# Optimization experiments

Measured on AMD Instinct MI355X. Metric: run time of the kernel, lower is better.

Reference implementation:

```python
import jax, jax.numpy as jnp
import numpy as np

POOL = 7  # RoIPooling output size (7,7)


def roi_pool(x, img, rois):
    """RoIPool matching the torch loop: scale rois to feature coords, truncate to int,
    take inclusive slice [y1:y2+1, x1:x2+1] and AdaptiveMaxPool2d((7,7)).
    x: [1,C,H,W], img: [1,3,h,w], rois: [N,4] (x1,y1,x2,y2 in image coords).
    Returns [N,C,7,7]."""
    _, C, H, W = x.shape
    h_img, w_img = img.shape[2], img.shape[3]
    scale = jnp.array([W / w_img, H / h_img, W / w_img, H / h_img], jnp.float32)
    r = (rois * scale).astype(jnp.int32)  # .long() truncation (coords >= 0)
    x1 = jnp.clip(r[:, 0], 0, W - 1)
    y1 = jnp.clip(r[:, 1], 0, H - 1)
    x2 = jnp.clip(r[:, 2], 0, W - 1)
    y2 = jnp.clip(r[:, 3], 0, H - 1)
    ww = x2 - x1 + 1  # inclusive slice width
    hh = y2 - y1 + 1
    i = jnp.arange(POOL)
    # AdaptiveMaxPool bin boundaries: start=floor(i*L/7), end=ceil((i+1)*L/7)  -> [N,7]
    col_s = x1[:, None] + (i[None, :] * ww[:, None]) // POOL
    col_e = x1[:, None] + ((i[None, :] + 1) * ww[:, None] + POOL - 1) // POOL
    row_s = y1[:, None] + (i[None, :] * hh[:, None]) // POOL
    row_e = y1[:, None] + ((i[None, :] + 1) * hh[:, None] + POOL - 1) // POOL
    wpos = jnp.arange(W)
    hpos = jnp.arange(H)
    colmask = (wpos[None, None, :] >= col_s[:, :, None]) & (wpos[None, None, :] < col_e[:, :, None])  # [N,7,W]
    rowmask = (hpos[None, None, :] >= row_s[:, :, None]) & (hpos[None, None, :] < row_e[:, :, None])  # [N,7,H]
    feat = x[0]  # [C,H,W]
    neg = jnp.asarray(jnp.finfo(feat.dtype).min, feat.dtype)
    def per_roi(masks):
        rm, cm = masks  # [7,H], [7,W]
        # separable max over the rectangular bin: cols first, then rows
        t = jnp.max(jnp.where(cm[None, None, :, :], feat[:, :, None, :], neg), axis=-1)  # [C,H,7]
        return jnp.max(jnp.where(rm[None, :, :, None], t[:, None, :, :], neg), axis=2)  # [C,7,7]
    return jax.lax.map(per_roi, (rowmask, colmask))  # [N,C,7,7]


def setup_inputs() -> dict:
    key = jax.random.key(0)
    ks = jax.random.split(key, 10)
    C, H, W = 512, 50, 50
    h_img, w_img = 800, 800
    N = 512
    num_classes = 20
    x = jax.random.normal(ks[0], (1, C, H, W), jnp.float32)
    img = jnp.zeros((1, 3, h_img, w_img), jnp.float32)
    bx = jax.random.uniform(ks[1], (N,), minval=0.0, maxval=w_img - 320.0)
    by = jax.random.uniform(ks[2], (N,), minval=0.0, maxval=h_img - 320.0)
    bw = jax.random.uniform(ks[3], (N,), minval=32.0, maxval=320.0)
    bh = jax.random.uniform(ks[4], (N,), minval=32.0, maxval=320.0)
    rois = jnp.stack([bx, by, bx + bw, by + bh], axis=1).astype(jnp.float32)
    D = C * POOL * POOL  # 25088
    W1 = jax.random.normal(ks[5], (D, 4096), jnp.float32) / np.sqrt(D)
    b1 = jnp.zeros((4096,), jnp.float32)
    W2 = jax.random.normal(ks[6], (4096, 4096), jnp.float32) / np.sqrt(4096)
    b2 = jnp.zeros((4096,), jnp.float32)
    Wcls = jax.random.normal(ks[7], (4096, num_classes + 1), jnp.float32) / np.sqrt(4096)
    bcls = jnp.zeros((num_classes + 1,), jnp.float32)
    Wreg = jax.random.normal(ks[8], (4096, 4 * (num_classes + 1)), jnp.float32) / np.sqrt(4096)
    breg = jnp.zeros((4 * (num_classes + 1),), jnp.float32)
    return {"x": x, "img": img, "rois": rois, "W1": W1, "b1": b1, "W2": W2,
            "b2": b2, "Wcls": Wcls, "bcls": bcls, "Wreg": Wreg, "breg": breg}


def reference(x, img, rois, W1, b1, W2, b2, Wcls, bcls, Wreg, breg):
    pooled = roi_pool(x, img, rois)                 # [N,C,7,7]
    f = pooled.reshape(pooled.shape[0], -1)          # flatten -> [N,25088]
    f = jax.nn.relu(f @ W1 + b1)                     # fc_head layer 1
    f = jax.nn.relu(f @ W2 + b2)                     # fc_head layer 2
    y_cls = f @ Wcls + bcls                          # [N, num_classes+1]
    y_reg = f @ Wreg + breg                          # [N, 4*(num_classes+1)]
    return (y_cls, y_reg)
```

## Files before the change

kernel.cpp:

```cpp
#include <hip/hip_runtime.h>


typedef __attribute__((ext_vector_type(8))) __bf16 bf16x8;
typedef __attribute__((ext_vector_type(4))) float f32x4;

#define N_ROIS 512
#define FH 50
#define FW 50
#define KK1 25088
#define D1 4096
#define BK 32

__device__ __forceinline__ void gll16(const void* g, void* l) {
  __builtin_amdgcn_global_load_lds(
      (const __attribute__((address_space(1))) void*)g,
      (__attribute__((address_space(3))) void*)l, 16, 0, 0);
}

__global__ __launch_bounds__(256) void roipool_kernel(
    const float* __restrict__ x, const float* __restrict__ rois,
    __bf16* __restrict__ pooled) {
  const int bid = blockIdx.x;
  const int roi = bid >> 3;
  const int cg = bid & 7;
  const float s = 0.0625f;
  const float r0 = rois[roi * 4 + 0], r1 = rois[roi * 4 + 1];
  const float r2 = rois[roi * 4 + 2], r3 = rois[roi * 4 + 3];
  int x1 = (int)(r0 * s); x1 = min(max(x1, 0), FW - 1);
  int y1 = (int)(r1 * s); y1 = min(max(y1, 0), FH - 1);
  int x2 = (int)(r2 * s); x2 = min(max(x2, 0), FW - 1);
  int y2 = (int)(r3 * s); y2 = min(max(y2, 0), FH - 1);
  const int ww = x2 - x1 + 1, hh = y2 - y1 + 1;
  __shared__ int cs[7], ce[7], rs[7], re[7];
  if (threadIdx.x < 7) {
    int i = threadIdx.x;
    cs[i] = x1 + (i * ww) / 7;
    ce[i] = x1 + ((i + 1) * ww + 6) / 7;
    rs[i] = y1 + (i * hh) / 7;
    re[i] = y1 + ((i + 1) * hh + 6) / 7;
  }
  __syncthreads();
  for (int idx = threadIdx.x; idx < 64 * 49; idx += 256) {
    int cl = idx / 49;
    int p = idx - cl * 49;
    int py = p / 7, px = p - py * 7;
    const int c = cg * 64 + cl;
    const float* base = x + (size_t)c * (FH * FW);
    float m = -3.402823466e38f;
    for (int y = rs[py]; y < re[py]; ++y) {
      const float* rowp = base + y * FW;
      for (int xx = cs[px]; xx < ce[px]; ++xx) m = fmaxf(m, rowp[xx]);
    }
    pooled[(size_t)roi * KK1 + c * 49 + p] = (__bf16)m;
  }
}

template <typename OutT>
__global__ __launch_bounds__(256, 1) void gemm_pipe(
    const __bf16* __restrict__ A, const float* __restrict__ B,
    OutT* __restrict__ part, int N, int K, int kslice, int npad, int zshift) {
  __shared__ float Blds[4][32 * 128];
  const int tid = threadIdx.x;
  const int lane = tid & 63;
  const int w = tid >> 6;
  const int bid = blockIdx.x;
  const int z = bid & ((1 << zshift) - 1);
  const int n0 = (bid >> zshift) * 128;
  const int kbeg = z * kslice;
  const int niters = kslice / BK;
  const int fr = lane & 15;
  const int ks = lane >> 4;

  f32x4 acc[8][8];
#pragma unroll
  for (int i = 0; i < 8; ++i)
#pragma unroll
    for (int j = 0; j < 8; ++j) acc[i][j] = (f32x4){0.f, 0.f, 0.f, 0.f};

  const __bf16* Abase = A + (size_t)(w * 128 + fr) * K + kbeg + ks * 8;
  const size_t Astride = (size_t)16 * K;

  const int srow = w * 8 + (lane >> 5);
  const float* Bsrc = B + n0 + (((lane & 31) ^ (2 * w)) << 2);

  bf16x8 afA[8], afB[8];

#define LOAD_A(D, t)                                                      \
  {                                                                       \
    int off = (t) * BK;                                                   \
    if (off >= kslice) off = 0;          \
    const __bf16* ap = Abase + off;                                       \
    _Pragma("unroll") for (int i = 0; i < 8; ++i)                         \
        D[i] = *(const bf16x8*)(ap + (size_t)i * Astride);                \
  }

#define STAGE(t)                                                          \
  {                                                                       \
    int off = (t) * BK;                                                   \
    if (off >= kslice) off = 0;    \
    _Pragma("unroll") for (int i = 0; i < 4; ++i) {                       \
      gll16((const void*)(Bsrc + (size_t)(kbeg + off + srow + 2 * i) * N),\
            (void*)&Blds[(t) & 3][(w * 8 + 2 * i) * 128]);                \
    }                                                                     \
  }

#define BODY(it, CA, NA)                                                  \
  {                                                                       \
    LOAD_A(NA, (it) + 1);                                                 \
    STAGE((it) + 2);                                                      \
    asm volatile("s_waitcnt vmcnt(16)" ::: "memory");                     \
    __builtin_amdgcn_s_barrier();                                         \
    __builtin_amdgcn_sched_barrier(0);                                    \
    const float* bl = &Blds[(it) & 3][0];                                 \
    _Pragma("unroll") for (int nf = 0; nf < 8; ++nf) {                    \
      const int base = (ks * 8) * 128 +                                   \
          (((nf * 4 + (fr >> 2)) ^ (2 * ks)) << 2) + (fr & 3);            \
      bf16x8 bfr;                                                         \
      _Pragma("unroll") for (int e = 0; e < 8; ++e)                       \
          bfr[e] = (__bf16)bl[base + e * 128];                            \
      _Pragma("unroll") for (int mf = 0; mf < 8; ++mf)                    \
          acc[mf][nf] = __builtin_amdgcn_mfma_f32_16x16x32_bf16(          \
              CA[mf], bfr, acc[mf][nf], 0, 0, 0);                         \
    }                                                                     \
  }

  STAGE(0);
  STAGE(1);
  LOAD_A(afA, 0);

  for (int it = 0; it < niters; it += 2) {
    BODY(it, afA, afB);
    BODY(it + 1, afB, afA);
  }
#undef BODY
#undef STAGE
#undef LOAD_A

  const int r0 = ks * 4;
  OutT* pbase = part + (size_t)z * 512 * npad;
#pragma unroll
  for (int mf = 0; mf < 8; ++mf)
#pragma unroll
    for (int nf = 0; nf < 8; ++nf) {
      const int col = n0 + nf * 16 + fr;
#pragma unroll
      for (int r = 0; r < 4; ++r) {
        const int row = w * 128 + mf * 16 + r0 + r;
        pbase[(size_t)row * npad + col] = (OutT)acc[mf][nf][r];
      }
    }
}

template <typename OutT>
__global__ __launch_bounds__(256, 1) void gemm_small(
    const __bf16* __restrict__ A, const float* __restrict__ B,
    OutT* __restrict__ part, int N, int K, int kslice, int npad, int zshift) {
  const int tid = threadIdx.x;
  const int lane = tid & 63;
  const int w = tid >> 6;
  const int bid = blockIdx.x;
  const int z = bid & ((1 << zshift) - 1);
  const int n0 = (bid >> zshift) * 64;
  const int kbeg = z * kslice;
  const int niters = kslice / BK;
  const int kmax = kbeg + kslice;
  const int fr = lane & 15;
  const int ks = lane >> 4;
  const int m0 = w * 128;
  const bool fullN = (n0 + 64) <= N;

  f32x4 acc[8][4];
#pragma unroll
  for (int i = 0; i < 8; ++i)
#pragma unroll
    for (int j = 0; j < 4; ++j) acc[i][j] = (f32x4){0.f, 0.f, 0.f, 0.f};

  const __bf16* Abase = A + (size_t)(m0 + fr) * K + ks * 8;
  const size_t Astride = (size_t)16 * K;
  const float* Bbase = B + n0 + fr;

  bf16x8 afA[8], afB[8];
  float bA[32], bB[32];

#define LOAD_A(D, t)                                                     \
  {                                                                      \
    int kk = kbeg + (t) * BK;                                            \
    if (kk >= kmax) kk = kbeg;                                           \
    const __bf16* ap = Abase + kk;                                       \
    _Pragma("unroll") for (int i = 0; i < 8; ++i)                        \
        D[i] = *(const bf16x8*)(ap + (size_t)i * Astride);               \
  }

#define LOAD_B(S, t)                                                     \
  {                                                                      \
    int kg = kbeg + (t) * BK;                                            \
    if (kg >= kmax) kg = kbeg;                                           \
    const float* p = Bbase + (size_t)(kg + ks * 8) * N;                  \
    if (fullN) {                                                         \
      _Pragma("unroll") for (int e = 0; e < 8; ++e) {                    \
        _Pragma("unroll") for (int nf = 0; nf < 4; ++nf)                 \
            S[e * 4 + nf] = p[nf * 16];                                  \
        p += N;                                                          \
      }                                                                  \
    } else {                                                             \
      _Pragma("unroll") for (int e = 0; e < 8; ++e) {                    \
        _Pragma("unroll") for (int nf = 0; nf < 4; ++nf)                 \
            S[e * 4 + nf] =                                              \
                (n0 + nf * 16 + fr < N) ? p[nf * 16] : 0.f;              \
        p += N;                                                          \
      }                                                                  \
    }                                                                    \
  }

#define BODY(it, CA, NA, CB)                                             \
  {                                                                      \
    bf16x8 bfr[4];                                                       \
    _Pragma("unroll") for (int e = 0; e < 8; ++e)                        \
        _Pragma("unroll") for (int nf = 0; nf < 4; ++nf)                 \
            bfr[nf][e] = (__bf16)CB[e * 4 + nf];                         \
    LOAD_B(CB, (it) + 2);                                                \
    LOAD_A(NA, (it) + 1);                                                \
    _Pragma("unroll") for (int nf = 0; nf < 4; ++nf)                     \
        _Pragma("unroll") for (int mf = 0; mf < 8; ++mf)                 \
            acc[mf][nf] = __builtin_amdgcn_mfma_f32_16x16x32_bf16(       \
                CA[mf], bfr[nf], acc[mf][nf], 0, 0, 0);                  \
  }

  LOAD_A(afA, 0);
  LOAD_B(bA, 0);
  LOAD_B(bB, 1);
  for (int it = 0; it < niters; it += 2) {
    BODY(it, afA, afB, bA);
    BODY(it + 1, afB, afA, bB);
  }
#undef BODY
#undef LOAD_B
#undef LOAD_A

  const int r0 = ks * 4;
  OutT* pbase = part + (size_t)z * 512 * npad;
#pragma unroll
  for (int mf = 0; mf < 8; ++mf)
#pragma unroll
    for (int nf = 0; nf < 4; ++nf) {
      const int col = n0 + nf * 16 + fr;
#pragma unroll
      for (int r = 0; r < 4; ++r) {
        const int row = m0 + mf * 16 + r0 + r;
        pbase[(size_t)row * npad + col] = (OutT)acc[mf][nf][r];
      }
    }
}

__global__ __launch_bounds__(256) void reduce_relu_kernel(
    const __bf16* __restrict__ part, const float* __restrict__ bias,
    __bf16* __restrict__ out, int nsplit) {
  const int idx = blockIdx.x * 256 + threadIdx.x;
  const int flat = idx * 8;
  if (flat >= 512 * 4096) return;
  float s[8];
#pragma unroll
  for (int j = 0; j < 8; ++j) s[j] = 0.f;
  for (int sp = 0; sp < nsplit; ++sp) {
    bf16x8 v = *(const bf16x8*)(part + (size_t)sp * (512 * 4096) + flat);
#pragma unroll
    for (int j = 0; j < 8; ++j) s[j] += (float)v[j];
  }
  const int nb = flat & 4095;
  bf16x8 o;
#pragma unroll
  for (int j = 0; j < 8; ++j) {
    float v = s[j] + bias[nb + j];
    o[j] = (__bf16)(v > 0.f ? v : 0.f);
  }
  *(bf16x8*)(out + flat) = o;
}

__global__ __launch_bounds__(256) void reduce_out_kernel(
    const float* __restrict__ pc, const float* __restrict__ pr,
    const float* __restrict__ bcls, const float* __restrict__ breg,
    float* __restrict__ out, int nsplit) {
  const int gid = blockIdx.x * 256 + threadIdx.x;
  if (gid >= 512 * 105) return;
  if (gid < 512 * 21) {
    const int m = gid / 21, j = gid - m * 21;
    float s = bcls[j];
    for (int sp = 0; sp < nsplit; ++sp)
      s += pc[(size_t)sp * 512 * 128 + m * 128 + j];
    out[gid] = s;
  } else {
    const int g = gid - 512 * 21;
    const int m = g / 84, j = g - m * 84;
    float s = breg[j];
    for (int sp = 0; sp < nsplit; ++sp)
      s += pr[(size_t)sp * 512 * 128 + m * 128 + j];
    out[gid] = s;
  }
}

extern "C" void kernel_launch(void* const* d_in, const int* in_sizes, int n_in,
                              void* d_out, int out_size, void* d_ws, size_t ws_size,
                              hipStream_t stream) {
  (void)in_sizes; (void)n_in; (void)out_size;
  const float* x    = (const float*)d_in[0];
  const float* rois = (const float*)d_in[2];
  const float* W1   = (const float*)d_in[3];
  const float* b1   = (const float*)d_in[4];
  const float* W2   = (const float*)d_in[5];
  const float* b2   = (const float*)d_in[6];
  const float* Wcls = (const float*)d_in[7];
  const float* bcls = (const float*)d_in[8];
  const float* Wreg = (const float*)d_in[9];
  const float* breg = (const float*)d_in[10];
  float* out = (float*)d_out;

  const size_t pooled_b = (size_t)512 * KK1 * 2;
  const size_t act_b = (size_t)512 * D1 * 2;
  const size_t need8 = pooled_b + (size_t)8 * act_b + 2 * act_b;
  const int ns = (ws_size >= need8) ? 8 : 2;
  const int zshift = (ns == 8) ? 3 : 1;

  char* ws = (char*)d_ws;
  __bf16* pooled = (__bf16*)ws;
  __bf16* part1 = (__bf16*)(ws + pooled_b);
  __bf16* f1 = (__bf16*)(ws + pooled_b + (size_t)ns * act_b);
  __bf16* f2 = (__bf16*)(ws + pooled_b + (size_t)ns * act_b + act_b);
  __bf16* part2 = (__bf16*)ws;
  float* pcls = (float*)ws;
  float* preg = (float*)(ws + (size_t)64 * 512 * 128 * 4);

  roipool_kernel<<<N_ROIS * 8, 256, 0, stream>>>(x, rois, pooled);

  gemm_pipe<__bf16><<<32 * ns, 256, 0, stream>>>(
      pooled, W1, part1, 4096, KK1, KK1 / ns, 4096, zshift);
  reduce_relu_kernel<<<1024, 256, 0, stream>>>(part1, b1, f1, ns);

  gemm_pipe<__bf16><<<32 * ns, 256, 0, stream>>>(
      f1, W2, part2, 4096, 4096, 4096 / ns, 4096, zshift);
  reduce_relu_kernel<<<1024, 256, 0, stream>>>(part2, b2, f2, ns);

  gemm_small<float><<<64, 256, 0, stream>>>(
      f2, Wcls, pcls, 21, 4096, 64, 128, 6);
  gemm_small<float><<<128, 256, 0, stream>>>(
      f2, Wreg, preg, 84, 4096, 64, 128, 6);
  reduce_out_kernel<<<(512 * 105 + 255) / 256, 256, 0, stream>>>(
      pcls, preg, bcls, breg, out, 64);
}
```

Measured before the change: 365.5 us.

## Stage A via LDS async loads and convert B to packed bf16 in registers

Reworks the gemm_pipe main loop. A tiles are now staged into double-buffered LDS with swizzled global_load_lds instead of direct register loads. B is loaded into registers as fp32, converted to bf16 and packed, then written to LDS in a transposed, swizzled layout so each B fragment is a single 16-byte LDS read. The goal is to avoid the eight scalar fp32 LDS reads plus per-element conversion for every B fragment, at the cost of more registers, more LDS, and an extra lgkmcnt wait in the pipeline.

```diff
diff --git a/kernel.cpp b/kernel.cpp
--- a/kernel.cpp
+++ b/kernel.cpp
@@ -3,6 +3,7 @@
 
 typedef __attribute__((ext_vector_type(8))) __bf16 bf16x8;
 typedef __attribute__((ext_vector_type(4))) float f32x4;
+typedef __attribute__((ext_vector_type(4))) unsigned int u32x4;
 
 #define N_ROIS 512
 #define FH 50
@@ -59,7 +60,8 @@
 __global__ __launch_bounds__(256, 1) void gemm_pipe(
     const __bf16* __restrict__ A, const float* __restrict__ B,
     OutT* __restrict__ part, int N, int K, int kslice, int npad, int zshift) {
-  __shared__ float Blds[4][32 * 128];
+  __shared__ unsigned int Bu[4][2048];
+  __shared__ __bf16 A_lds[2][512 * 32];
   const int tid = threadIdx.x;
   const int lane = tid & 63;
   const int w = tid >> 6;
@@ -77,64 +79,116 @@
 #pragma unroll
     for (int j = 0; j < 8; ++j) acc[i][j] = (f32x4){0.f, 0.f, 0.f, 0.f};
 
-  const __bf16* Abase = A + (size_t)(w * 128 + fr) * K + kbeg + ks * 8;
-  const size_t Astride = (size_t)16 * K;
-
-  const int srow = w * 8 + (lane >> 5);
-  const float* Bsrc = B + n0 + (((lane & 31) ^ (2 * w)) << 2);
-
-  bf16x8 afA[8], afB[8];
-
-#define LOAD_A(D, t)                                                      \
-  {                                                                       \
-    int off = (t) * BK;                                                   \
-    if (off >= kslice) off = 0;          \
-    const __bf16* ap = Abase + off;                                       \
-    _Pragma("unroll") for (int i = 0; i < 8; ++i)                         \
-        D[i] = *(const bf16x8*)(ap + (size_t)i * Astride);                \
-  }
-
-#define STAGE(t)                                                          \
+  const int aswz = (lane & 3) ^ ((lane >> 2) & 3) ^ ((lane >> 4) & 3);
+  const __bf16* Asrc =
+      A + (size_t)(w * 128 + (lane >> 2)) * K + kbeg + aswz * 8;
+  const int aslot = ks ^ ((fr & 3) ^ ((fr >> 2) & 3));
+
+  const int bc = tid & 127;
+  const int bh = tid >> 7;
+  const float* Bgsrc = B + n0 + bc;
+  const int bswz = (bc >> 2) & 3;
+  const int widx0 = bc * 16 + (((2 * bh) ^ bswz) << 2);
+  const int widx1 = bc * 16 + (((2 * bh + 1) ^ bswz) << 2);
+
+  bf16x8 af[8];
+  float gA0, gA1, gA2, gA3, gA4, gA5, gA6, gA7,
+        gA8, gA9, gAa, gAb, gAc, gAd, gAe, gAf;
+  float gB0, gB1, gB2, gB3, gB4, gB5, gB6, gB7,
+        gB8, gB9, gBa, gBb, gBc, gBd, gBe, gBf;
+
+#define STAGE_A(t)                                                        \
   {                                                                       \
     int off = (t) * BK;                                                   \
     if (off >= kslice) off = 0;    \
-    _Pragma("unroll") for (int i = 0; i < 4; ++i) {                       \
-      gll16((const void*)(Bsrc + (size_t)(kbeg + off + srow + 2 * i) * N),\
-            (void*)&Blds[(t) & 3][(w * 8 + 2 * i) * 128]);                \
+    _Pragma("unroll") for (int i = 0; i < 8; ++i) {                       \
+      gll16((const void*)(Asrc + (size_t)(i * 16) * K + off),             \
+            (void*)&A_lds[(t) & 1][(w * 128 + i * 16) * 32]);             \
     }                                                                     \
   }
 
-#define BODY(it, CA, NA)                                                  \
+#define LOAD_BG(S, t)                                                     \
   {                                                                       \
-    LOAD_A(NA, (it) + 1);                                                 \
-    STAGE((it) + 2);                                                      \
-    asm volatile("s_waitcnt vmcnt(16)" ::: "memory");                     \
+    int off = (t) * BK;                                                   \
+    if (off >= kslice) off = 0;             \
+    const float* p = Bgsrc + (size_t)(kbeg + off + 16 * bh) * N;          \
+    S##0 = p[0];            S##1 = p[(size_t)N];                          \
+    S##2 = p[(size_t)2*N];  S##3 = p[(size_t)3*N];                        \
+    S##4 = p[(size_t)4*N];  S##5 = p[(size_t)5*N];                        \
+    S##6 = p[(size_t)6*N];  S##7 = p[(size_t)7*N];                        \
+    S##8 = p[(size_t)8*N];  S##9 = p[(size_t)9*N];                        \
+    S##a = p[(size_t)10*N]; S##b = p[(size_t)11*N];                       \
+    S##c = p[(size_t)12*N]; S##d = p[(size_t)13*N];                       \
+    S##e = p[(size_t)14*N]; S##f = p[(size_t)15*N];                       \
+  }
+
+#define PK(lo, hi)                                                        \
+  ((unsigned int)(__bf16_raw{(__bf16)(lo)}.x) |                           \
+   ((unsigned int)(__bf16_raw{(__bf16)(hi)}.x) << 16))
+
+#define WRITE_BU(buf, S)                                                  \
+  {                                                                       \
+    union { __bf16 h[2]; unsigned int u; } q;                             \
+    unsigned int u0, u1, u2, u3, u4, u5, u6, u7;                          \
+    q.h[0] = (__bf16)S##0; q.h[1] = (__bf16)S##1; u0 = q.u;               \
+    q.h[0] = (__bf16)S##2; q.h[1] = (__bf16)S##3; u1 = q.u;               \
+    q.h[0] = (__bf16)S##4; q.h[1] = (__bf16)S##5; u2 = q.u;               \
+    q.h[0] = (__bf16)S##6; q.h[1] = (__bf16)S##7; u3 = q.u;               \
+    q.h[0] = (__bf16)S##8; q.h[1] = (__bf16)S##9; u4 = q.u;               \
+    q.h[0] = (__bf16)S##a; q.h[1] = (__bf16)S##b; u5 = q.u;               \
+    q.h[0] = (__bf16)S##c; q.h[1] = (__bf16)S##d; u6 = q.u;               \
+    q.h[0] = (__bf16)S##e; q.h[1] = (__bf16)S##f; u7 = q.u;               \
+    *(u32x4*)&Bu[buf][widx0] = (u32x4){u0, u1, u2, u3};                   \
+    *(u32x4*)&Bu[buf][widx1] = (u32x4){u4, u5, u6, u7};                   \
+  }
+
+  LOAD_BG(gA, 0);
+  LOAD_BG(gB, 1);
+  STAGE_A(0);
+  WRITE_BU(0, gA);
+
+#define BODY(it, WRS, LDS_)                                               \
+  {                                                                       \
+    if ((it) + 1 < niters) WRITE_BU(((it) + 1) & 3, WRS);                 \
+    LOAD_BG(LDS_, (it) + 2);                                              \
+    STAGE_A((it) + 1);                                                    \
+    asm volatile("s_waitcnt vmcnt(24)" ::: "memory");                     \
+    asm volatile("s_waitcnt lgkmcnt(0)" ::: "memory");                    \
     __builtin_amdgcn_s_barrier();                                         \
     __builtin_amdgcn_sched_barrier(0);                                    \
-    const float* bl = &Blds[(it) & 3][0];                                 \
+    {                                                                     \
+      const __bf16* al = &A_lds[(it) & 1][0];                             \
+      _Pragma("unroll") for (int mf = 0; mf < 8; ++mf)                    \
+          af[mf] = *(const bf16x8*)(al + (w * 128 + mf * 16 + fr) * 32 +  \
+                                    aslot * 8);                           \
+    }                                                                     \
+    const unsigned int* bl = &Bu[(it) & 3][0];                            \
+    bf16x8 bf0, bf1;                                                      \
+    bf0 = *(const bf16x8*)((const char*)bl +                              \
+                           (0 * 16 + fr) * 64 + (ks ^ ((fr >> 2) & 3)) * 16); \
     _Pragma("unroll") for (int nf = 0; nf < 8; ++nf) {                    \
-      const int base = (ks * 8) * 128 +                                   \
-          (((nf * 4 + (fr >> 2)) ^ (2 * ks)) << 2) + (fr & 3);            \
-      bf16x8 bfr;                                                         \
-      _Pragma("unroll") for (int e = 0; e < 8; ++e)                       \
-          bfr[e] = (__bf16)bl[base + e * 128];                            \
+      const int c_ = nf * 16 + fr;                                        \
+      if (nf + 1 < 8) {                                                   \
+        const int cn_ = (nf + 1) * 16 + fr;                               \
+        bf1 = *(const bf16x8*)((const char*)bl + cn_ * 64 +               \
+                               (ks ^ ((cn_ >> 2) & 3)) * 16);             \
+      }                                                                   \
+      (void)c_;                                                           \
       _Pragma("unroll") for (int mf = 0; mf < 8; ++mf)                    \
           acc[mf][nf] = __builtin_amdgcn_mfma_f32_16x16x32_bf16(          \
-              CA[mf], bfr, acc[mf][nf], 0, 0, 0);                         \
+              af[mf], bf0, acc[mf][nf], 0, 0, 0);                         \
+      bf0 = bf1;                                                          \
     }                                                                     \
   }
 
-  STAGE(0);
-  STAGE(1);
-  LOAD_A(afA, 0);
-
   for (int it = 0; it < niters; it += 2) {
-    BODY(it, afA, afB);
-    BODY(it + 1, afB, afA);
+    BODY(it, gB, gA);
+    BODY(it + 1, gA, gB);
   }
 #undef BODY
-#undef STAGE
-#undef LOAD_A
+#undef WRITE_BU
+#undef LOAD_BG
+#undef STAGE_A
 
   const int r0 = ks * 4;
   OutT* pbase = part + (size_t)z * 512 * npad;
```

Result: slower. 402.3 us (+10.1%).
